# Performance work log

Hardware: AMD Instinct MI355X
Metric: run time of the kernel (lower is better)

## Reference

```python
import jax, jax.numpy as jnp
import numpy as np

HEAD = 16
NEG = -1.0e9


def setup_inputs() -> dict:
    key = jax.random.key(0)
    ks = jax.random.split(key, 8)
    B, S, D = 2, 2048, 1024
    scale = 1.0 / np.sqrt(D)
    inp = {
        "query": jax.random.normal(ks[0], (B, S, D), jnp.float32),
        "key": jax.random.normal(ks[1], (B, S, D), jnp.float32),
        "value": jax.random.normal(ks[2], (B, S, D), jnp.float32),
        "mask": jnp.ones((B, S, S), jnp.int32),
        "w_q": jax.random.normal(ks[3], (D, D), jnp.float32) * scale,
        "b_q": jnp.zeros((D,), jnp.float32),
        "w_k": jax.random.normal(ks[4], (D, D), jnp.float32) * scale,
        "b_k": jnp.zeros((D,), jnp.float32),
        "w_v": jax.random.normal(ks[5], (D, D), jnp.float32) * scale,
        "b_v": jnp.zeros((D,), jnp.float32),
        "w_o": jax.random.normal(ks[6], (D, D), jnp.float32) * scale,
        "b_o": jnp.zeros((D,), jnp.float32),
    }
    return inp


def _split_heads(x, B, S, H, dk):
    # [B,S,D] -> [B,H,S,dk]
    return x.reshape(B, S, H, dk).transpose(0, 2, 1, 3)


def reference(query, key, value, mask, w_q, b_q, w_k, b_k, w_v, b_v, w_o, b_o):
    B, S, D = query.shape
    H = HEAD
    dk = D // H
    q = _split_heads(query @ w_q.T + b_q, B, S, H, dk)
    k = _split_heads(key @ w_k.T + b_k, B, S, H, dk)
    v = _split_heads(value @ w_v.T + b_v, B, S, H, dk)
    # scores: [B,H,S,S]
    scores = jnp.einsum('bhqd,bhkd->bhqk', q, k) / jnp.sqrt(jnp.float32(dk))
    scores = jnp.where(mask[:, None, :, :] == 0, NEG, scores)
    p = jax.nn.softmax(scores, axis=-1)  # dropout is identity in eval
    x = jnp.einsum('bhqk,bhkd->bhqd', p, v)  # [B,H,S,dk]
    x = x.transpose(0, 2, 1, 3).reshape(B, S, D)
    return x @ w_o.T + b_o
```

## Files before the change

kernel.cpp:

```cpp
#include <hip/hip_runtime.h>
#include <hip/hip_bf16.h>

typedef float f32x4 __attribute__((ext_vector_type(4)));
typedef short bf16x8 __attribute__((ext_vector_type(8)));
typedef unsigned short u16x4 __attribute__((ext_vector_type(4)));

#define BB 2
#define SS 2048
#define DM 1024
#define NH 16
#define DKH 64
#define MROWS 4096

__device__ __forceinline__ unsigned short f2bf(float x) {
  union { float f; unsigned int u; } v; v.f = x;
  unsigned int r = v.u + 0x7fffu + ((v.u >> 16) & 1u);
  return (unsigned short)(r >> 16);
}

__device__ __forceinline__ void gll16(const void* g, void* l) {
  __builtin_amdgcn_global_load_lds(
      (const __attribute__((address_space(1))) void*)g,
      (__attribute__((address_space(3))) void*)l, 16, 0, 0);
}

template <int C>
__device__ __forceinline__ float dppf(float x) {
  return __builtin_bit_cast(float,
      __builtin_amdgcn_mov_dpp(__builtin_bit_cast(int, x), C, 0xf, 0xf, true));
}
__device__ __forceinline__ float rowsum16(float v) {
  v += dppf<0xB1>(v);
  v += dppf<0x4E>(v);
  v += dppf<0x141>(v);
  v += dppf<0x140>(v);
  return v;
}

struct CvtArgs {
  const float* src[7];
  unsigned short* dst[7];
  const int* mask;
  int* flags;
};

__global__ __launch_bounds__(256) void cvt_mask_kernel(CvtArgs a) {
  const int bid = blockIdx.x;
  if (bid >= 16384) {
    const int mb = bid - 16384;
    const int b = mb >> 8, qt = (mb >> 4) & 15, kt = mb & 15;
    __shared__ int sf;
    if (threadIdx.x == 0) sf = 0;
    __syncthreads();
    int any0 = 0;
    const size_t base = ((size_t)b * SS + qt * 128) * SS + kt * 128;
    for (int p = 0; p < 64; ++p) {
      int i = p * 256 + threadIdx.x;
      int r = i >> 7, col = i & 127;
      any0 |= (a.mask[base + (size_t)r * SS + col] == 0);
    }
    if (any0) sf = 1;
    __syncthreads();
    if (threadIdx.x == 0) a.flags[mb] = sf;
    return;
  }
  int z, i;
  if (bid < 12288) { z = bid >> 12; i = (bid & 4095) * 256 + threadIdx.x; }
  else { z = 3 + ((bid - 12288) >> 10); i = ((bid - 12288) & 1023) * 256 + threadIdx.x; }
  f32x4 v = ((const f32x4*)a.src[z])[i];
  u16x4 o;
  o[0] = f2bf(v[0]); o[1] = f2bf(v[1]); o[2] = f2bf(v[2]); o[3] = f2bf(v[3]);
  ((u16x4*)a.dst[z])[i] = o;
}

struct ProjArgs {
  const unsigned short* A[3];
  const unsigned short* W[3];
  const float* bias[3];
  void* out[3];
  float alpha[3];
  int mode[3];
};

template <int TAG, int MT>
__global__ __launch_bounds__(256, 3) void proj_gemm(ProjArgs args) {
  constexpr int NI = MT / 32;
  constexpr int PBUF = MT * 128 + 16384;
  __shared__ __align__(16) char pbuf[PBUF];
  unsigned short (*As)[64] = (unsigned short (*)[64])pbuf;
  unsigned short (*Bs)[64] = (unsigned short (*)[64])(pbuf + MT * 128);
  unsigned short (*T)[136] = (unsigned short (*)[136])pbuf;

  const int z = blockIdx.z;
  const unsigned short* __restrict__ A = args.A[z];
  const unsigned short* __restrict__ W = args.W[z];
  const float* __restrict__ bias = args.bias[z];
  const float alpha = args.alpha[z];
  const int mode = args.mode[z];

  const int tid = threadIdx.x;
  const int w = tid >> 6, lane = tid & 63;
  const int quad = lane >> 4, c = lane & 15;
  const int m0 = blockIdx.x * MT, n0 = blockIdx.y * 128;
  const int wm = (w >> 1) * (MT / 2), wn = (w & 1) * 64;
  const int s8r = lane >> 3, s8c = lane & 7;
  const int g8 = (s8c ^ s8r) * 8;
  const int cx = c & 7;

  f32x4 acc[NI][4];
#pragma unroll
  for (int i = 0; i < NI; ++i)
#pragma unroll
    for (int j = 0; j < 4; ++j) { f32x4 zz = {0.f, 0.f, 0.f, 0.f}; acc[i][j] = zz; }

  for (int kt = 0; kt < 16; ++kt) {
    const int k0 = kt * 64;
    __syncthreads();
#pragma unroll
    for (int t = 0; t < MT / 32; ++t) {
      const int r = (w * (MT / 32) + t) * 8 + s8r;
      gll16(A + (size_t)(m0 + r) * DM + k0 + g8, &As[r][s8c * 8]);
    }
#pragma unroll
    for (int t = 0; t < 4; ++t) {
      const int r = (w * 4 + t) * 8 + s8r;
      gll16(W + (size_t)(n0 + r) * DM + k0 + g8, &Bs[r][s8c * 8]);
    }
    __syncthreads();
#pragma unroll
    for (int kk = 0; kk < 2; ++kk) {
      const int po = ((quad ^ cx) ^ (kk * 4)) * 8;
      bf16x8 af[NI], bfr[4];
#pragma unroll
      for (int i = 0; i < NI; ++i) af[i] = *(const bf16x8*)&As[wm + i * 16 + c][po];
#pragma unroll
      for (int j = 0; j < 4; ++j) bfr[j] = *(const bf16x8*)&Bs[wn + j * 16 + c][po];
#pragma unroll
      for (int i = 0; i < NI; ++i)
#pragma unroll
        for (int j = 0; j < 4; ++j)
          acc[i][j] = __builtin_amdgcn_mfma_f32_16x16x32_bf16(af[i], bfr[j], acc[i][j], 0, 0, 0);
    }
  }

  if constexpr (MT == 128) {
    if (mode == 1) {
      unsigned short* outp = (unsigned short*)args.out[z];
      const int bb = m0 >> 11, sblk = (m0 >> 7) & 15;
#pragma unroll
      for (int h = 0; h < 2; ++h) {
        __syncthreads();
        if ((w & 1) == h) {
#pragma unroll
          for (int j = 0; j < 4; ++j) {
            const int row = j * 16 + c;
            const float bn = bias[n0 + h * 64 + row];
#pragma unroll
            for (int r = 0; r < 4; ++r) {
              u16x4 pkt;
#pragma unroll
              for (int i = 0; i < 4; ++i) pkt[i] = f2bf((acc[i][j][r] + bn) * alpha);
              *(u16x4*)&T[row][quad * 32 + r * 8 + (w >> 1) * 4] = pkt;
            }
          }
        }
        __syncthreads();
        const int row = tid >> 2, seg = tid & 3;
        const int n = n0 + h * 64 + row;
        const int hh = n >> 6, d = n & 63;
        const size_t gb = (((size_t)(bb * NH + hh)) * DKH + d) * SS + sblk * 128;
#pragma unroll
        for (int q = 0; q < 4; ++q)
          *(bf16x8*)&outp[gb + (seg + 4 * q) * 8] = *(const bf16x8*)&T[row][(seg + 4 * q) * 8];
      }
      return;
    }
  }

#pragma unroll
  for (int i = 0; i < NI; ++i)
#pragma unroll
    for (int j = 0; j < 4; ++j)
#pragma unroll
      for (int r = 0; r < 4; ++r) {
        const int m = m0 + wm + i * 16 + quad * 4 + r;
        const int n = n0 + wn + j * 16 + c;
        const float val = (acc[i][j][r] + bias[n]) * alpha;
        if (mode == 2) {
          ((float*)args.out[z])[(size_t)m * DM + n] = val;
        } else {
          const int bb = m >> 11, s = m & 2047, hh = n >> 6, d = n & 63;
          const size_t idx = (((size_t)(bb * NH + hh)) * SS + s) * DKH + d;
          ((unsigned short*)args.out[z])[idx] = f2bf(val);
        }
      }
}

__global__ __launch_bounds__(256, 2) void attn_kernel(
    const unsigned short* __restrict__ qp, const unsigned short* __restrict__ kp,
    const unsigned short* __restrict__ vtp, const int* __restrict__ mask,
    const int* __restrict__ flags, unsigned short* __restrict__ xb) {
  __shared__ __align__(16) char smem[65536];
  unsigned short (*Ks)[128][32] = (unsigned short (*)[128][32])smem;
  unsigned short (*Vt)[64][32]  = (unsigned short (*)[64][32])(smem + 16384);
  unsigned short (*Qs)[128][32] = (unsigned short (*)[128][32])(smem + 32768);
  unsigned short (*Ps)[128]     = (unsigned short (*)[128])(smem + 32768);

  const int tid = threadIdx.x;
  const int w = tid >> 6, lane = tid & 63;
  const int quad = lane >> 4, c = lane & 15;
  const int qt = blockIdx.x, bh = blockIdx.y;
  const int b = bh >> 4, h = bh & 15;
  const int q0 = qt * 128;
  const int sr = lane >> 2, scc = lane & 3;
  const int lx = scc ^ ((sr >> 1) & 3);
  const int sk = (quad ^ ((c >> 1) & 3)) * 8;

#pragma unroll
  for (int t = 0; t < 4; ++t) {
    const int tt = w * 4 + t;
    const int kk = tt >> 3;
    const int r = (tt & 7) * 16 + sr;
    gll16(qp + ((size_t)bh * SS + q0 + r) * DKH + kk * 32 + lx * 8, &Qs[kk][r][scc * 8]);
  }
  __syncthreads();
  bf16x8 aq[2][2];
#pragma unroll
  for (int rt = 0; rt < 2; ++rt)
#pragma unroll
    for (int kk = 0; kk < 2; ++kk)
      aq[rt][kk] = *(const bf16x8*)&Qs[kk][w * 32 + rt * 16 + c][sk];

  f32x4 acco[2][4];
#pragma unroll
  for (int rt = 0; rt < 2; ++rt)
#pragma unroll
    for (int j = 0; j < 4; ++j) { f32x4 zz = {0.f, 0.f, 0.f, 0.f}; acco[rt][j] = zz; }
  float l_run[2][4];
#pragma unroll
  for (int rt = 0; rt < 2; ++rt)
#pragma unroll
    for (int r = 0; r < 4; ++r) l_run[rt][r] = 0.f;

  for (int kt = 0; kt < 16; ++kt) {
    const int k0 = kt * 128;
    __syncthreads();
#pragma unroll
    for (int i = 0; i < 4; ++i) {
      const int tt = w * 4 + i;
      {
        const int kk = tt >> 3, r = (tt & 7) * 16 + sr;
        gll16(kp + ((size_t)bh * SS + k0 + r) * DKH + kk * 32 + lx * 8, &Ks[kk][r][scc * 8]);
      }
      {
        const int kc = tt >> 2, d = (tt & 3) * 16 + sr;
        gll16(vtp + ((size_t)bh * DKH + d) * SS + k0 + kc * 32 + lx * 8, &Vt[kc][d][scc * 8]);
      }
    }
    __syncthreads();

    f32x4 accs[2][8];
#pragma unroll
    for (int rt = 0; rt < 2; ++rt)
#pragma unroll
      for (int j = 0; j < 8; ++j) { f32x4 zz = {0.f, 0.f, 0.f, 0.f}; accs[rt][j] = zz; }
#pragma unroll
    for (int j = 0; j < 8; ++j) {
      const int rowk = j * 16 + c;
      const bf16x8 bk0 = *(const bf16x8*)&Ks[0][rowk][sk];
      const bf16x8 bk1 = *(const bf16x8*)&Ks[1][rowk][sk];
#pragma unroll
      for (int rt = 0; rt < 2; ++rt) {
        accs[rt][j] = __builtin_amdgcn_mfma_f32_16x16x32_bf16(aq[rt][0], bk0, accs[rt][j], 0, 0, 0);
        accs[rt][j] = __builtin_amdgcn_mfma_f32_16x16x32_bf16(aq[rt][1], bk1, accs[rt][j], 0, 0, 0);
      }
    }

    if (flags[((size_t)b * 16 + qt) * 16 + kt]) {
#pragma unroll
      for (int rt = 0; rt < 2; ++rt)
#pragma unroll
        for (int j = 0; j < 8; ++j)
#pragma unroll
          for (int r = 0; r < 4; ++r) {
            const int qq = q0 + w * 32 + rt * 16 + quad * 4 + r;
            const int kk2 = k0 + j * 16 + c;
            if (mask[((size_t)b * SS + qq) * SS + kk2] == 0) accs[rt][j][r] = -1.0e30f;
          }
    }

#pragma unroll
    for (int rt = 0; rt < 2; ++rt)
#pragma unroll
      for (int r = 0; r < 4; ++r) {
        union { bf16x8 v8; __hip_bfloat162 h2[4]; } pk;
        float s = 0.f;
#pragma unroll
        for (int jj = 0; jj < 4; ++jj) {
          const float p0 = __builtin_amdgcn_exp2f(accs[rt][2 * jj][r]);
          const float p1 = __builtin_amdgcn_exp2f(accs[rt][2 * jj + 1][r]);
          float2 pp; pp.x = p0; pp.y = p1;
          pk.h2[jj] = __float22bfloat162_rn(pp);
          s += p0 + p1;
        }
        l_run[rt][r] += s;
        const int prow = w * 32 + rt * 16 + quad * 4 + r;
        *(bf16x8*)&Ps[prow][(c ^ ((prow >> 1) & 7)) * 8] = pk.v8;
      }

#pragma unroll
    for (int kc = 0; kc < 4; ++kc) {
      const int pc = ((kc * 4 + quad) ^ ((c >> 1) & 7)) * 8;
      const bf16x8 ap0 = *(const bf16x8*)&Ps[w * 32 + c][pc];
      const bf16x8 ap1 = *(const bf16x8*)&Ps[w * 32 + 16 + c][pc];
#pragma unroll
      for (int j = 0; j < 4; ++j) {
        const bf16x8 bv = *(const bf16x8*)&Vt[kc][j * 16 + c][sk];
        acco[0][j] = __builtin_amdgcn_mfma_f32_16x16x32_bf16(ap0, bv, acco[0][j], 0, 0, 0);
        acco[1][j] = __builtin_amdgcn_mfma_f32_16x16x32_bf16(ap1, bv, acco[1][j], 0, 0, 0);
      }
    }
  }

#pragma unroll
  for (int rt = 0; rt < 2; ++rt)
#pragma unroll
    for (int r = 0; r < 4; ++r) {
      const float inv = 1.0f / rowsum16(l_run[rt][r]);
      const int q = q0 + w * 32 + rt * 16 + quad * 4 + r;
#pragma unroll
      for (int j = 0; j < 4; ++j) {
        xb[((size_t)b * SS + q) * DM + h * DKH + j * 16 + c] = f2bf(acco[rt][j][r] * inv);
      }
    }
}

extern "C" void kernel_launch(void* const* d_in, const int* in_sizes, int n_in,
                              void* d_out, int out_size, void* d_ws, size_t ws_size,
                              hipStream_t stream) {
  (void)in_sizes; (void)n_in; (void)out_size; (void)ws_size;
  const float* query = (const float*)d_in[0];
  const float* key_  = (const float*)d_in[1];
  const float* value = (const float*)d_in[2];
  const int*   mask  = (const int*)d_in[3];
  const float* w_q = (const float*)d_in[4];
  const float* b_q = (const float*)d_in[5];
  const float* w_k = (const float*)d_in[6];
  const float* b_k = (const float*)d_in[7];
  const float* w_v = (const float*)d_in[8];
  const float* b_v = (const float*)d_in[9];
  const float* w_o = (const float*)d_in[10];
  const float* b_o = (const float*)d_in[11];

  char* ws = (char*)d_ws;
  const size_t SZ_IN = (size_t)MROWS * DM * 2;
  const size_t SZ_W  = (size_t)DM * DM * 2;
  unsigned short* qin = (unsigned short*)(ws);
  unsigned short* kin = (unsigned short*)(ws + SZ_IN);
  unsigned short* vin = (unsigned short*)(ws + 2 * SZ_IN);
  unsigned short* wqb = (unsigned short*)(ws + 3 * SZ_IN);
  unsigned short* wkb = (unsigned short*)(ws + 3 * SZ_IN + SZ_W);
  unsigned short* wvb = (unsigned short*)(ws + 3 * SZ_IN + 2 * SZ_W);
  unsigned short* wob = (unsigned short*)(ws + 3 * SZ_IN + 3 * SZ_W);
  unsigned short* qp  = (unsigned short*)(ws + 3 * SZ_IN + 4 * SZ_W);
  unsigned short* kp  = (unsigned short*)(ws + 4 * SZ_IN + 4 * SZ_W);
  unsigned short* vtp = (unsigned short*)(ws + 5 * SZ_IN + 4 * SZ_W);
  unsigned short* xb  = (unsigned short*)(ws + 6 * SZ_IN + 4 * SZ_W);
  int* flags          = (int*)(ws + 7 * SZ_IN + 4 * SZ_W);

  CvtArgs ca;
  ca.src[0] = query; ca.src[1] = key_; ca.src[2] = value;
  ca.src[3] = w_q; ca.src[4] = w_k; ca.src[5] = w_v; ca.src[6] = w_o;
  ca.dst[0] = qin; ca.dst[1] = kin; ca.dst[2] = vin;
  ca.dst[3] = wqb; ca.dst[4] = wkb; ca.dst[5] = wvb; ca.dst[6] = wob;
  ca.mask = mask; ca.flags = flags;
  cvt_mask_kernel<<<dim3(16896), 256, 0, stream>>>(ca);

  ProjArgs pa;
  pa.A[0] = qin; pa.A[1] = kin; pa.A[2] = vin;
  pa.W[0] = wqb; pa.W[1] = wkb; pa.W[2] = wvb;
  pa.bias[0] = b_q; pa.bias[1] = b_k; pa.bias[2] = b_v;
  pa.out[0] = qp; pa.out[1] = kp; pa.out[2] = vtp;
  pa.alpha[0] = 0.18033688011112042f; pa.alpha[1] = 1.f; pa.alpha[2] = 1.f;
  pa.mode[0] = 0; pa.mode[1] = 0; pa.mode[2] = 1;
  proj_gemm<0, 128><<<dim3(32, 8, 3), 256, 0, stream>>>(pa);

  attn_kernel<<<dim3(16, 32), 256, 0, stream>>>(qp, kp, vtp, mask, flags, xb);

  ProjArgs po;
  po.A[0] = po.A[1] = po.A[2] = xb;
  po.W[0] = po.W[1] = po.W[2] = wob;
  po.bias[0] = po.bias[1] = po.bias[2] = b_o;
  po.out[0] = po.out[1] = po.out[2] = d_out;
  po.alpha[0] = po.alpha[1] = po.alpha[2] = 1.f;
  po.mode[0] = po.mode[1] = po.mode[2] = 2;
  proj_gemm<1, 64><<<dim3(64, 8, 1), 256, 0, stream>>>(po);
}
```

Measured before the change: 254.3 us.

## Remap projection GEMM tiles per XCD and interleave QK^T with exp packing

The projection GEMM now remaps its linear block id so that blocks dispatched to the same XCD cover a compact rectangle of output tiles. This is meant to improve L2 reuse of A and W rows on the multi-XCD MI355X. In attention, the score MFMAs for each 16-column slice are immediately followed by masking, exp2 and bf16 packing instead of first accumulating all 8 slices. That shrinks live registers from the full score tile to packed words and lets exp work overlap MFMA latency. The flag load is also hoisted before the barrier.

```diff
diff --git a/kernel.cpp b/kernel.cpp
--- a/kernel.cpp
+++ b/kernel.cpp
@@ -101,7 +101,18 @@
   const int tid = threadIdx.x;
   const int w = tid >> 6, lane = tid & 63;
   const int quad = lane >> 4, c = lane & 15;
-  const int m0 = blockIdx.x * MT, n0 = blockIdx.y * 128;
+  constexpr int GX = (MT == 128) ? 32 : 64;
+  const int id = blockIdx.x + GX * blockIdx.y;
+  const int xcd = id & 7, sl = id >> 3;
+  int bx, by;
+  if constexpr (MT == 128) {
+    bx = (xcd & 3) * 8 + (sl & 7);
+    by = (xcd >> 2) * 4 + (sl >> 3);
+  } else {
+    bx = (xcd & 3) * 16 + (sl & 15);
+    by = (xcd >> 2) * 4 + (sl >> 4);
+  }
+  const int m0 = bx * MT, n0 = by * 128;
   const int wm = (w >> 1) * (MT / 2), wn = (w & 1) * 64;
   const int s8r = lane >> 3, s8c = lane & 7;
   const int g8 = (s8c ^ s8r) * 8;
@@ -257,55 +268,55 @@
         gll16(vtp + ((size_t)bh * DKH + d) * SS + k0 + kc * 32 + lx * 8, &Vt[kc][d][scc * 8]);
       }
     }
-    __syncthreads();
-
-    f32x4 accs[2][8];
-#pragma unroll
-    for (int rt = 0; rt < 2; ++rt)
-#pragma unroll
-      for (int j = 0; j < 8; ++j) { f32x4 zz = {0.f, 0.f, 0.f, 0.f}; accs[rt][j] = zz; }
+    const int flagv = flags[((size_t)b * 16 + qt) * 16 + kt];
+    __syncthreads();
+
+    unsigned int pkw[2][4][4];
+    float pprev[2][4];
 #pragma unroll
     for (int j = 0; j < 8; ++j) {
       const int rowk = j * 16 + c;
       const bf16x8 bk0 = *(const bf16x8*)&Ks[0][rowk][sk];
       const bf16x8 bk1 = *(const bf16x8*)&Ks[1][rowk][sk];
+      f32x4 sj[2];
 #pragma unroll
       for (int rt = 0; rt < 2; ++rt) {
-        accs[rt][j] = __builtin_amdgcn_mfma_f32_16x16x32_bf16(aq[rt][0], bk0, accs[rt][j], 0, 0, 0);
-        accs[rt][j] = __builtin_amdgcn_mfma_f32_16x16x32_bf16(aq[rt][1], bk1, accs[rt][j], 0, 0, 0);
-      }
-    }
-
-    if (flags[((size_t)b * 16 + qt) * 16 + kt]) {
-#pragma unroll
-      for (int rt = 0; rt < 2; ++rt)
-#pragma unroll
-        for (int j = 0; j < 8; ++j)
+        f32x4 zz = {0.f, 0.f, 0.f, 0.f};
+        zz = __builtin_amdgcn_mfma_f32_16x16x32_bf16(aq[rt][0], bk0, zz, 0, 0, 0);
+        sj[rt] = __builtin_amdgcn_mfma_f32_16x16x32_bf16(aq[rt][1], bk1, zz, 0, 0, 0);
+      }
+      if (flagv) {
+#pragma unroll
+        for (int rt = 0; rt < 2; ++rt)
 #pragma unroll
           for (int r = 0; r < 4; ++r) {
             const int qq = q0 + w * 32 + rt * 16 + quad * 4 + r;
             const int kk2 = k0 + j * 16 + c;
-            if (mask[((size_t)b * SS + qq) * SS + kk2] == 0) accs[rt][j][r] = -1.0e30f;
+            if (mask[((size_t)b * SS + qq) * SS + kk2] == 0) sj[rt][r] = -1.0e30f;
           }
-    }
-
+      }
+#pragma unroll
+      for (int rt = 0; rt < 2; ++rt)
+#pragma unroll
+        for (int r = 0; r < 4; ++r) {
+          const float p = __builtin_amdgcn_exp2f(sj[rt][r]);
+          l_run[rt][r] += p;
+          if (j & 1) {
+            float2 pp; pp.x = pprev[rt][r]; pp.y = p;
+            const __hip_bfloat162 h2 = __float22bfloat162_rn(pp);
+            union { __hip_bfloat162 h; unsigned int u; } cv; cv.h = h2;
+            pkw[rt][r][j >> 1] = cv.u;
+          } else {
+            pprev[rt][r] = p;
+          }
+        }
+    }
 #pragma unroll
     for (int rt = 0; rt < 2; ++rt)
 #pragma unroll
       for (int r = 0; r < 4; ++r) {
-        union { bf16x8 v8; __hip_bfloat162 h2[4]; } pk;
-        float s = 0.f;
-#pragma unroll
-        for (int jj = 0; jj < 4; ++jj) {
-          const float p0 = __builtin_amdgcn_exp2f(accs[rt][2 * jj][r]);
-          const float p1 = __builtin_amdgcn_exp2f(accs[rt][2 * jj + 1][r]);
-          float2 pp; pp.x = p0; pp.y = p1;
-          pk.h2[jj] = __float22bfloat162_rn(pp);
-          s += p0 + p1;
-        }
-        l_run[rt][r] += s;
         const int prow = w * 32 + rt * 16 + quad * 4 + r;
-        *(bf16x8*)&Ps[prow][(c ^ ((prow >> 1) & 7)) * 8] = pk.v8;
+        *(bf16x8*)&Ps[prow][(c ^ ((prow >> 1) & 7)) * 8] = *(const bf16x8*)&pkw[rt][r][0];
       }
 
 #pragma unroll
```

New measurement: 262.7 us. 1.03x slower.
